# Kernel optimization log

Hardware: AMD Instinct MI355X
Metric: run time of the kernel (lower is better)

The kernel has to match this reference:

```python
import jax, jax.numpy as jnp
import numpy as np

B, T_IN, D = 16, 512, 384
MAX_LEN = 2048


def setup_inputs() -> dict:
    key = jax.random.key(0)
    k1, k2 = jax.random.split(key)
    x = jax.random.normal(k1, (B, T_IN, D), dtype=jnp.float32)
    durations = jax.random.randint(k2, (B, T_IN), 0, 10).astype(jnp.int32)
    return {"x": x, "durations": durations, "max_len": MAX_LEN}


def reference(x, durations, max_len):
    # reps = (durations.float() + 0.5).long()  -> round-half-up to int frames
    reps = jnp.floor(durations.astype(jnp.float32) + 0.5).astype(jnp.int32)  # [B, T_in]
    dec_lens = reps.sum(axis=1)  # [B]
    # cumulative durations, padded with leading 0: [B, 1, T_in+1]
    reps_cumsum = jnp.cumsum(
        jnp.pad(reps, ((0, 0), (1, 0))), axis=1
    ).astype(x.dtype)[:, None, :]
    # frame index grid r: [1, L, 1] (static length == max_len; original uses
    # dec_lens.max() then slices to max_len — identical when max_len <= dec_lens.max())
    r = jnp.arange(max_len, dtype=x.dtype)[None, :, None]
    # boolean interval-membership matrix: frame t belongs to phoneme i iff
    # cum[i] <= t < cum[i+1]
    mult = ((reps_cumsum[:, :, :-1] <= r) & (reps_cumsum[:, :, 1:] > r)).astype(x.dtype)  # [B, L, T_in]
    out = jnp.matmul(mult, x)  # [B, L, D]
    dec_lens = jnp.minimum(dec_lens, jnp.asarray(max_len, dec_lens.dtype))
    return out, dec_lens
```

## Files before the change

kernel.cpp:

```cpp
#include <hip/hip_runtime.h>

#define B_ 16
#define T_IN_ 512
#define D_ 384
#define MAX_LEN_ 2048
#define D4_ (D_ / 4)

__global__ __launch_bounds__(T_IN_) void lr_scan_kernel(
    const int* __restrict__ durations,
    int* __restrict__ idx_map,
    float* __restrict__ dec_lens_out)
{
    const int b = blockIdx.x;
    const int tid = threadIdx.x;

    __shared__ int s[T_IN_];

    for (int t = tid; t < MAX_LEN_; t += T_IN_)
        idx_map[b * MAX_LEN_ + t] = -1;

    const int dur = durations[b * T_IN_ + tid];
    const int rep = (int)floorf((float)dur + 0.5f);

    s[tid] = rep;
    __syncthreads();

    #pragma unroll
    for (int off = 1; off < T_IN_; off <<= 1) {
        int v = (tid >= off) ? s[tid - off] : 0;
        __syncthreads();
        s[tid] += v;
        __syncthreads();
    }

    const int incl = s[tid];
    const int excl = incl - rep;
    const int end  = min(incl, MAX_LEN_);

    for (int t = excl; t < end; ++t)
        idx_map[b * MAX_LEN_ + t] = tid;

    if (tid == 0) {
        const int total = s[T_IN_ - 1];
        dec_lens_out[b] = (float)min(total, MAX_LEN_);
    }
}

__global__ __launch_bounds__(256) void lr_gather_kernel(
    const float4* __restrict__ x4,
    const int* __restrict__ idx_map,
    float4* __restrict__ out4)
{
    const int total = B_ * MAX_LEN_ * D4_;
    const int stride = gridDim.x * blockDim.x;
    for (int n = blockIdx.x * blockDim.x + threadIdx.x; n < total; n += stride) {
        const int d4   = n % D4_;
        const int rest = n / D4_;
        const int t    = rest % MAX_LEN_;
        const int b    = rest / MAX_LEN_;

        const int ph = idx_map[b * MAX_LEN_ + t];
        float4 v = make_float4(0.f, 0.f, 0.f, 0.f);
        if (ph >= 0)
            v = x4[(b * T_IN_ + ph) * D4_ + d4];
        out4[n] = v;
    }
}

extern "C" void kernel_launch(void* const* d_in, const int* in_sizes, int n_in,
                              void* d_out, int out_size, void* d_ws, size_t ws_size,
                              hipStream_t stream) {
    const float* x         = (const float*)d_in[0];
    const int*   durations = (const int*)d_in[1];

    float* out      = (float*)d_out;
    float* dec_lens = (float*)d_out + (size_t)B_ * MAX_LEN_ * D_;
    int*   idx_map  = (int*)d_ws;

    lr_scan_kernel<<<B_, T_IN_, 0, stream>>>(durations, idx_map, dec_lens);

    const int total4 = B_ * MAX_LEN_ * D4_;
    const int block = 256;
    const int grid = 2048;
    (void)total4; (void)in_sizes; (void)n_in; (void)out_size; (void)ws_size;
    lr_gather_kernel<<<grid, block, 0, stream>>>(
        (const float4*)x, idx_map, (float4*)out);
}
```

Measured before the change: 84.15 us.

## Fuse duration scan and gather into one kernel with per-block binary search

Merges the two kernels into one. Each block redoes the prefix sum of its batch's 512 durations in shared memory, then finds the phoneme index for each of its 32 frames by binary search. This removes the second launch, the idx_map round trip through global memory, and the serial per-thread fill loop. In exchange every one of the 1024 blocks repeats the 512-element scan, which is redundant work and extra synchronisation per block. It also drops the floor(+0.5) rounding, which is harmless for integer durations.

```diff
diff --git a/kernel.cpp b/kernel.cpp
--- a/kernel.cpp
+++ b/kernel.cpp
@@ -4,66 +4,65 @@
 #define T_IN_ 512
 #define D_ 384
 #define MAX_LEN_ 2048
-#define D4_ (D_ / 4)
+#define D4_ 96
+#define FRAMES_PER_BLOCK 32
+#define BLOCKS_PER_BATCH (MAX_LEN_ / FRAMES_PER_BLOCK)
+#define F4_PER_BLOCK (FRAMES_PER_BLOCK * D4_)
+#define ITERS (F4_PER_BLOCK / 256)
 
-__global__ __launch_bounds__(T_IN_) void lr_scan_kernel(
+__global__ __launch_bounds__(256) void lr_fused_kernel(
+    const float4* __restrict__ x4,
     const int* __restrict__ durations,
-    int* __restrict__ idx_map,
-    float* __restrict__ dec_lens_out)
+    float4* __restrict__ out4,
+    float* __restrict__ dec_lens)
 {
-    const int b = blockIdx.x;
-    const int tid = threadIdx.x;
+    __shared__ int s[T_IN_];
+    __shared__ int sph[FRAMES_PER_BLOCK];
 
-    __shared__ int s[T_IN_];
+    const int tid        = threadIdx.x;
+    const int b          = blockIdx.x / BLOCKS_PER_BATCH;
+    const int chunk      = blockIdx.x % BLOCKS_PER_BATCH;
+    const int frame_base = chunk * FRAMES_PER_BLOCK;
 
-    for (int t = tid; t < MAX_LEN_; t += T_IN_)
-        idx_map[b * MAX_LEN_ + t] = -1;
-
-    const int dur = durations[b * T_IN_ + tid];
-    const int rep = (int)floorf((float)dur + 0.5f);
-
-    s[tid] = rep;
+    s[tid]       = durations[b * T_IN_ + tid];
+    s[tid + 256] = durations[b * T_IN_ + tid + 256];
     __syncthreads();
 
     #pragma unroll
     for (int off = 1; off < T_IN_; off <<= 1) {
-        int v = (tid >= off) ? s[tid - off] : 0;
+        const int i0 = tid, i1 = tid + 256;
+        const int v0 = (i0 >= off) ? s[i0 - off] : 0;
+        const int v1 = (i1 >= off) ? s[i1 - off] : 0;
         __syncthreads();
-        s[tid] += v;
+        s[i0] += v0;
+        s[i1] += v1;
         __syncthreads();
     }
 
-    const int incl = s[tid];
-    const int excl = incl - rep;
-    const int end  = min(incl, MAX_LEN_);
+    if (tid < FRAMES_PER_BLOCK) {
+        const int t = frame_base + tid;
+        int lo = 0, hi = T_IN_;
+        #pragma unroll
+        for (int it = 0; it < 9; ++it) {
+            const int mid = (lo + hi) >> 1;
+            if (s[mid] > t) hi = mid; else lo = mid + 1;
+        }
+        sph[tid] = (lo < T_IN_) ? lo : -1;
+    }
+    if (chunk == 0 && tid == 0)
+        dec_lens[b] = (float)min(s[T_IN_ - 1], MAX_LEN_);
+    __syncthreads();
 
-    for (int t = excl; t < end; ++t)
-        idx_map[b * MAX_LEN_ + t] = tid;
-
-    if (tid == 0) {
-        const int total = s[T_IN_ - 1];
-        dec_lens_out[b] = (float)min(total, MAX_LEN_);
-    }
-}
-
-__global__ __launch_bounds__(256) void lr_gather_kernel(
-    const float4* __restrict__ x4,
-    const int* __restrict__ idx_map,
-    float4* __restrict__ out4)
-{
-    const int total = B_ * MAX_LEN_ * D4_;
-    const int stride = gridDim.x * blockDim.x;
-    for (int n = blockIdx.x * blockDim.x + threadIdx.x; n < total; n += stride) {
-        const int d4   = n % D4_;
-        const int rest = n / D4_;
-        const int t    = rest % MAX_LEN_;
-        const int b    = rest / MAX_LEN_;
-
-        const int ph = idx_map[b * MAX_LEN_ + t];
-        float4 v = make_float4(0.f, 0.f, 0.f, 0.f);
-        if (ph >= 0)
-            v = x4[(b * T_IN_ + ph) * D4_ + d4];
-        out4[n] = v;
+    const float4 zero = make_float4(0.f, 0.f, 0.f, 0.f);
+    const size_t out_base = ((size_t)b * MAX_LEN_ + frame_base) * D4_;
+    const size_t x_base   = (size_t)b * T_IN_ * D4_;
+    #pragma unroll
+    for (int j = 0; j < ITERS; ++j) {
+        const int k  = tid + j * 256;
+        const int tl = k / D4_;
+        const int d4 = k - tl * D4_;
+        const int ph = sph[tl];
+        out4[out_base + k] = (ph >= 0) ? x4[x_base + (size_t)ph * D4_ + d4] : zero;
     }
 }
 
@@ -75,14 +74,9 @@
 
     float* out      = (float*)d_out;
     float* dec_lens = (float*)d_out + (size_t)B_ * MAX_LEN_ * D_;
-    int*   idx_map  = (int*)d_ws;
 
-    lr_scan_kernel<<<B_, T_IN_, 0, stream>>>(durations, idx_map, dec_lens);
+    (void)in_sizes; (void)n_in; (void)out_size; (void)d_ws; (void)ws_size;
 
-    const int total4 = B_ * MAX_LEN_ * D4_;
-    const int block = 256;
-    const int grid = 2048;
-    (void)total4; (void)in_sizes; (void)n_in; (void)out_size; (void)ws_size;
-    lr_gather_kernel<<<grid, block, 0, stream>>>(
-        (const float4*)x, idx_map, (float4*)out);
+    lr_fused_kernel<<<B_ * BLOCKS_PER_BATCH, 256, 0, stream>>>(
+        (const float4*)x, durations, (float4*)out, dec_lens);
 }
```

Result: faster. 81.82 us (-2.8%).
